# Performance work log

Measured on AMD Instinct MI355X. Metric: run time of the kernel, lower is better.

## Reference

```python
import jax, jax.numpy as jnp
import numpy as np

B, S, DIM = 2, 2048, 2048
N_HEADS, N_KV_HEADS = 32, 8
HEAD_DIM = DIM // N_HEADS  # 64
N_REP = N_HEADS // N_KV_HEADS  # 4
ROPE_THETA = 10000.0


def setup_inputs() -> dict:
    key = jax.random.key(0)
    ks = jax.random.split(key, 5)
    x = jax.random.normal(ks[0], (B, S, DIM), dtype=jnp.float32)
    # rope frequencies: freqs_cis[t, j] = exp(i * t * theta^(-2j/head_dim))
    inv_freq = 1.0 / (ROPE_THETA ** (jnp.arange(0, HEAD_DIM, 2, dtype=jnp.float32) / HEAD_DIM))
    angles = jnp.arange(S, dtype=jnp.float32)[:, None] * inv_freq[None, :]  # [S, HEAD_DIM//2]
    freqs_cos = jnp.cos(angles)
    freqs_sin = jnp.sin(angles)
    scale = 1.0 / np.sqrt(DIM)
    wq = jax.random.normal(ks[1], (N_HEADS * HEAD_DIM, DIM), dtype=jnp.float32) * scale
    wk = jax.random.normal(ks[2], (N_KV_HEADS * HEAD_DIM, DIM), dtype=jnp.float32) * scale
    wv = jax.random.normal(ks[3], (N_KV_HEADS * HEAD_DIM, DIM), dtype=jnp.float32) * scale
    wo = jax.random.normal(ks[4], (DIM, N_HEADS * HEAD_DIM), dtype=jnp.float32) * scale
    return {"x": x, "freqs_cos": freqs_cos, "freqs_sin": freqs_sin,
            "wq": wq, "wk": wk, "wv": wv, "wo": wo}


def _rope(t, cos, sin):
    # t: [B, S, H, D]; rotate consecutive pairs (even, odd) lanes -- complex mul.
    t = t.reshape(*t.shape[:-1], HEAD_DIM // 2, 2)
    t0, t1 = t[..., 0], t[..., 1]
    c = cos[None, :, None, :]  # [1, S, 1, D//2]
    s = sin[None, :, None, :]
    r0 = t0 * c - t1 * s
    r1 = t0 * s + t1 * c
    return jnp.stack([r0, r1], axis=-1).reshape(*t0.shape[:-1], HEAD_DIM)


def reference(x, freqs_cos, freqs_sin, wq, wk, wv, wo):
    bsz, seqlen, _ = x.shape
    xq = jnp.einsum('bsd,hd->bsh', x, wq).reshape(bsz, seqlen, N_HEADS, HEAD_DIM)
    xk = jnp.einsum('bsd,hd->bsh', x, wk).reshape(bsz, seqlen, N_KV_HEADS, HEAD_DIM)
    xv = jnp.einsum('bsd,hd->bsh', x, wv).reshape(bsz, seqlen, N_KV_HEADS, HEAD_DIM)
    xq = _rope(xq, freqs_cos[:seqlen], freqs_sin[:seqlen])
    xk = _rope(xk, freqs_cos[:seqlen], freqs_sin[:seqlen])
    # GQA: repeat_interleave kv heads to n_heads
    xk = jnp.repeat(xk, N_REP, axis=2)
    xv = jnp.repeat(xv, N_REP, axis=2)
    # [B, H, S, D]
    q = xq.transpose(0, 2, 1, 3)
    k = xk.transpose(0, 2, 1, 3)
    v = xv.transpose(0, 2, 1, 3)
    scores = jnp.einsum('bhqd,bhkd->bhqk', q, k) / np.sqrt(HEAD_DIM)
    causal = jnp.tril(jnp.ones((seqlen, seqlen), dtype=bool))
    scores = jnp.where(causal[None, None], scores, jnp.finfo(scores.dtype).min)
    attn = jax.nn.softmax(scores, axis=-1)
    out = jnp.einsum('bhqk,bhkd->bhqd', attn, v)
    out = out.transpose(0, 2, 1, 3).reshape(bsz, seqlen, N_HEADS * HEAD_DIM)
    return jnp.einsum('bsh,dh->bsd', out, wo)
```

## Files before the change

### kernel.cpp

```cpp
#include <hip/hip_runtime.h>
#include <hip/hip_bf16.h>
#include <stdint.h>

#define BATCH 2
#define SEQ   2048
#define DIM   2048
#define NH    32
#define NKV   8
#define HD    64
#define QKVN  3072
#define MROWS 4096

typedef __bf16 bf16x8 __attribute__((ext_vector_type(8)));
typedef float  f32x4  __attribute__((ext_vector_type(4)));
typedef unsigned short ushort8v __attribute__((ext_vector_type(8)));

typedef __attribute__((address_space(3))) void lds_void;
typedef const __attribute__((address_space(1))) void gbl_void;

__device__ __forceinline__ void gload_lds16(const void* g, void* l) {
    __builtin_amdgcn_global_load_lds((gbl_void*)g, (lds_void*)l, 16, 0, 0);
}

__global__ void cvt_f32_bf16(const float* __restrict__ in,
                             __hip_bfloat16* __restrict__ out, int n) {
    int i = (blockIdx.x * 256 + threadIdx.x) * 4;
    if (i >= n) return;
    const float4 v = *reinterpret_cast<const float4*>(in + i);
    union { ushort4 u; __hip_bfloat16 h[4]; } o;
    o.h[0] = __float2bfloat16(v.x);
    o.h[1] = __float2bfloat16(v.y);
    o.h[2] = __float2bfloat16(v.z);
    o.h[3] = __float2bfloat16(v.w);
    *reinterpret_cast<ushort4*>(out + i) = o.u;
}

__device__ __forceinline__ void store_out(float* p, float v) { *p = v; }
__device__ __forceinline__ void store_out(__hip_bfloat16* p, float v) { *p = __float2bfloat16(v); }

template <typename OUT_T>
__global__ __launch_bounds__(256) void gemm_bt(
    const __hip_bfloat16* __restrict__ A,
    const __hip_bfloat16* __restrict__ B,
    OUT_T* __restrict__ C,
    int M, int N, int K)
{
    __shared__ __align__(16) __hip_bfloat16 As[128 * 32];
    __shared__ __align__(16) __hip_bfloat16 Bs[128 * 32];
    const int tid  = threadIdx.x;
    const int lane = tid & 63;
    const int wave = tid >> 6;
    const int wr = wave >> 1, wc = wave & 1;
    const int lr = lane & 15, lg = lane >> 4;

    const int nwg = (int)(gridDim.x * gridDim.y);
    const int id  = (int)blockIdx.y * (int)gridDim.x + (int)blockIdx.x;
    const int cpx = nwg >> 3;
    const int sw  = (id & 7) * cpx + (id >> 3);
    const size_t tm = (size_t)(sw % (int)gridDim.x) * 128;
    const size_t tn = (size_t)(sw / (int)gridDim.x) * 128;

    f32x4 acc[4][4] = {};

    const int srow  = tid >> 2;
    const int scol  = (tid & 3) * 8;
    const int wbase = wave * 512;

    const __hip_bfloat16* pa = As + (wr * 64 + lr) * 32 + lg * 8;
    const __hip_bfloat16* pb = Bs + (wc * 64 + lr) * 32 + lg * 8;

    for (int k0 = 0; k0 < K; k0 += 32) {
        const __hip_bfloat16* gA = A + (tm + srow) * (size_t)K + k0 + scol;
        const __hip_bfloat16* gB = B + (tn + srow) * (size_t)K + k0 + scol;
        gload_lds16(gA,                 (void*)(As + wbase));
        gload_lds16(gA + (size_t)64*K,  (void*)(As + 2048 + wbase));
        gload_lds16(gB,                 (void*)(Bs + wbase));
        gload_lds16(gB + (size_t)64*K,  (void*)(Bs + 2048 + wbase));
        __syncthreads();
        bf16x8 af[4], bfr[4];
        #pragma unroll
        for (int m = 0; m < 4; ++m) af[m]  = *reinterpret_cast<const bf16x8*>(pa + m * 512);
        #pragma unroll
        for (int n = 0; n < 4; ++n) bfr[n] = *reinterpret_cast<const bf16x8*>(pb + n * 512);
        #pragma unroll
        for (int m = 0; m < 4; ++m)
            #pragma unroll
            for (int n = 0; n < 4; ++n)
                acc[m][n] = __builtin_amdgcn_mfma_f32_16x16x32_bf16(af[m], bfr[n], acc[m][n], 0, 0, 0);
        __syncthreads();
    }

    #pragma unroll
    for (int m = 0; m < 4; ++m)
        #pragma unroll
        for (int n = 0; n < 4; ++n)
            #pragma unroll
            for (int r = 0; r < 4; ++r) {
                size_t row = tm + wr * 64 + m * 16 + lg * 4 + r;
                size_t col = tn + wc * 64 + n * 16 + lr;
                store_out(&C[row * (size_t)N + col], acc[m][n][r]);
            }
}

__global__ void rope_qk(const __hip_bfloat16* __restrict__ qkv,
                        const float* __restrict__ fcos,
                        const float* __restrict__ fsin,
                        __hip_bfloat16* __restrict__ outp,
                        int nheads, int col_off, float mul) {
    int idx = blockIdx.x * 256 + threadIdx.x;
    int i  = idx & 31;
    int s  = (idx >> 5) & (SEQ - 1);
    int bh = idx >> 16;
    int h  = bh % nheads;
    const __hip_bfloat16* src = qkv + ((size_t)(bh / nheads) * SEQ + s) * QKVN
                                    + col_off + h * HD + 2 * i;
    union { unsigned int u; __hip_bfloat16 h2[2]; } in_, out_;
    in_.u = *reinterpret_cast<const unsigned int*>(src);
    float t0 = __bfloat162float(in_.h2[0]);
    float t1 = __bfloat162float(in_.h2[1]);
    float c  = fcos[s * 32 + i] * mul;
    float sn = fsin[s * 32 + i] * mul;
    out_.h2[0] = __float2bfloat16(t0 * c - t1 * sn);
    out_.h2[1] = __float2bfloat16(t0 * sn + t1 * c);
    *reinterpret_cast<unsigned int*>(outp + ((size_t)bh * SEQ + s) * HD + 2 * i) = out_.u;
}

__global__ __launch_bounds__(256) void v_repack(const __hip_bfloat16* __restrict__ qkv,
                                                __hip_bfloat16* __restrict__ vt) {
    __shared__ unsigned short tile[64][66];
    int blk = blockIdx.x;
    int st = blk & 31;
    int kh = (blk >> 5) & 7;
    int b  = blk >> 8;
    int s0 = st * 64;
    int t  = threadIdx.x;
    int r  = t >> 2;
    #pragma unroll
    for (int it = 0; it < 2; ++it) {
        int chunk = (t & 3) + it * 4;
        const __hip_bfloat16* src = qkv + ((size_t)(b * SEQ + s0 + r)) * QKVN
                                        + 2560 + kh * HD + chunk * 8;
        ushort8v v = *reinterpret_cast<const ushort8v*>(src);
        #pragma unroll
        for (int j = 0; j < 8; ++j) tile[r][chunk * 8 + j] = v[j];
    }
    __syncthreads();
    int d = t >> 2;
    #pragma unroll
    for (int it = 0; it < 2; ++it) {
        int chunk = (t & 3) + it * 4;
        ushort8v w;
        #pragma unroll
        for (int j = 0; j < 8; ++j) w[j] = tile[chunk * 8 + j][d];
        *reinterpret_cast<ushort8v*>(vt + ((size_t)(b * NKV + kh) * HD + d) * SEQ
                                        + s0 + chunk * 8) = w;
    }
}

__device__ __forceinline__ unsigned pack_bf16x2(float lo, float hi) {
    __hip_bfloat162 t;
    t.x = __float2bfloat16(lo);
    t.y = __float2bfloat16(hi);
    return *reinterpret_cast<unsigned*>(&t);
}

__global__ __launch_bounds__(256, 4) void flash_attn(
    const __hip_bfloat16* __restrict__ Qp,
    const __hip_bfloat16* __restrict__ Kp,
    const __hip_bfloat16* __restrict__ Vt,
    __hip_bfloat16* __restrict__ O) {
    __shared__ __align__(16) __hip_bfloat16 Kst[2][4096];
    __shared__ __align__(16) __hip_bfloat16 Vst[2][4096];
    __shared__ __align__(16) unsigned char Plds[4][2048];
    const int qt   = (int)gridDim.x - 1 - (int)blockIdx.x;
    const int bh   = blockIdx.y;
    const int b    = bh >> 5, h = bh & 31;
    const int kvh  = h >> 2;
    const int tid  = threadIdx.x;
    const int wave = tid >> 6, lane = tid & 63;
    const int lr = lane & 15, lg = lane >> 4;
    const int qw0 = qt * 64 + wave * 16;

    const __hip_bfloat16* qbase = Qp + (((size_t)bh) * SEQ + qw0 + lr) * HD + lg * 8;
    const bf16x8 qa0 = *reinterpret_cast<const bf16x8*>(qbase);
    const bf16x8 qa1 = *reinterpret_cast<const bf16x8*>(qbase + 32);

    const __hip_bfloat16* kb = Kp + ((size_t)(b * NKV + kvh) * SEQ) * HD;
    const __hip_bfloat16* vb = Vt + ((size_t)(b * NKV + kvh) * HD) * SEQ;

    const int srow = tid >> 3;
    const int sch  = (tid & 7) ^ (srow & 7);
    const size_t koff0 = (size_t)srow        * HD  + sch * 8;
    const size_t koff1 = (size_t)(srow + 32) * HD  + sch * 8;
    const size_t voff0 = (size_t)srow        * SEQ + sch * 8;
    const size_t voff1 = (size_t)(srow + 32) * SEQ + sch * 8;
    const int wvb = wave * 1024;

    int foff[4][2];
    #pragma unroll
    for (int g = 0; g < 4; ++g)
        #pragma unroll
        for (int c = 0; c < 2; ++c)
            foff[g][c] = (g * 16 + lr) * 64 + (((c * 4 + lg) ^ (lr & 7)) * 8);

    f32x4 acc[4] = {};
    float m_run = -1e30f;
    float l_run = 0.f;

    unsigned char* pw = &Plds[wave][0];
    const int swz = (lr & 7) << 4;
    const int kv_end = qt * 64 + 64;

    {
        char* kd = (char*)&Kst[0][0];
        char* vd = (char*)&Vst[0][0];
        gload_lds16(kb + koff0, kd + wvb);
        gload_lds16(kb + koff1, kd + 4096 + wvb);
        gload_lds16(vb + voff0, vd + wvb);
        gload_lds16(vb + voff1, vd + 4096 + wvb);
    }
    int cur = 0;

    for (int kv0 = 0; kv0 < kv_end; kv0 += 64) {
        __syncthreads();
        if (kv0 + 64 < kv_end) {
            const __hip_bfloat16* ks = kb + (size_t)(kv0 + 64) * HD;
            const __hip_bfloat16* vs = vb + (kv0 + 64);
            char* kd = (char*)&Kst[cur ^ 1][0];
            char* vd = (char*)&Vst[cur ^ 1][0];
            gload_lds16(ks + koff0, kd + wvb);
            gload_lds16(ks + koff1, kd + 4096 + wvb);
            gload_lds16(vs + voff0, vd + wvb);
            gload_lds16(vs + voff1, vd + 4096 + wvb);
        }
        const __hip_bfloat16* Kl = &Kst[cur][0];
        const __hip_bfloat16* Vl = &Vst[cur][0];

        f32x4 s[4];
        #pragma unroll
        for (int nk = 0; nk < 4; ++nk) {
            bf16x8 k0 = *reinterpret_cast<const bf16x8*>(Kl + foff[nk][0]);
            bf16x8 k1 = *reinterpret_cast<const bf16x8*>(Kl + foff[nk][1]);
            f32x4 z = {0.f, 0.f, 0.f, 0.f};
            z = __builtin_amdgcn_mfma_f32_16x16x32_bf16(k0, qa0, z, 0, 0, 0);
            z = __builtin_amdgcn_mfma_f32_16x16x32_bf16(k1, qa1, z, 0, 0, 0);
            s[nk] = z;
        }
        if (kv0 + 64 >= kv_end) {
            const int qg = qw0 + lr;
            #pragma unroll
            for (int nk = 0; nk < 4; ++nk) {
                const int kbase = kv0 + nk * 16 + lg * 4;
                #pragma unroll
                for (int r = 0; r < 4; ++r)
                    if (kbase + r > qg) s[nk][r] = -1e30f;
            }
        }
        float pmax = fmaxf(fmaxf(s[0][0], s[0][1]), fmaxf(s[0][2], s[0][3]));
        #pragma unroll
        for (int nk = 1; nk < 4; ++nk)
            pmax = fmaxf(pmax, fmaxf(fmaxf(s[nk][0], s[nk][1]), fmaxf(s[nk][2], s[nk][3])));
        if (!__all(pmax - m_run <= 8.0f)) {
            float tmax = fmaxf(pmax, __shfl_xor(pmax, 16, 64));
            tmax = fmaxf(tmax, __shfl_xor(tmax, 32, 64));
            const float mn    = fmaxf(m_run, tmax);
            const float alpha = __expf(m_run - mn);
            m_run = mn;
            l_run *= alpha;
            const float a0 = __shfl(alpha, lg * 4 + 0, 64);
            const float a1 = __shfl(alpha, lg * 4 + 1, 64);
            const float a2 = __shfl(alpha, lg * 4 + 2, 64);
            const float a3 = __shfl(alpha, lg * 4 + 3, 64);
            #pragma unroll
            for (int nd = 0; nd < 4; ++nd) {
                acc[nd][0] *= a0; acc[nd][1] *= a1;
                acc[nd][2] *= a2; acc[nd][3] *= a3;
            }
        }
        float tsum = 0.f;
        #pragma unroll
        for (int nk = 0; nk < 4; ++nk) {
            float p0 = __expf(s[nk][0] - m_run);
            float p1 = __expf(s[nk][1] - m_run);
            float p2 = __expf(s[nk][2] - m_run);
            float p3 = __expf(s[nk][3] - m_run);
            tsum += (p0 + p1) + (p2 + p3);
            uint2 pk;
            pk.x = pack_bf16x2(p0, p1);
            pk.y = pack_bf16x2(p2, p3);
            *reinterpret_cast<uint2*>(pw + lr * 128 + ((nk * 32 + lg * 8) ^ swz)) = pk;
        }
        l_run += tsum;
        asm volatile("s_waitcnt lgkmcnt(0)" ::: "memory");
        __builtin_amdgcn_sched_barrier(0);
        const bf16x8 pa0 = *reinterpret_cast<const bf16x8*>(pw + lr * 128 + ((     lg * 16) ^ swz));
        const bf16x8 pa1 = *reinterpret_cast<const bf16x8*>(pw + lr * 128 + ((64 + lg * 16) ^ swz));
        #pragma unroll
        for (int nd = 0; nd < 4; ++nd) {
            bf16x8 v0 = *reinterpret_cast<const bf16x8*>(Vl + foff[nd][0]);
            bf16x8 v1 = *reinterpret_cast<const bf16x8*>(Vl + foff[nd][1]);
            acc[nd] = __builtin_amdgcn_mfma_f32_16x16x32_bf16(pa0, v0, acc[nd], 0, 0, 0);
            acc[nd] = __builtin_amdgcn_mfma_f32_16x16x32_bf16(pa1, v1, acc[nd], 0, 0, 0);
        }
        cur ^= 1;
    }
    float lt = l_run;
    lt += __shfl_xor(lt, 16, 64);
    lt += __shfl_xor(lt, 32, 64);
    float linv[4];
    #pragma unroll
    for (int r = 0; r < 4; ++r)
        linv[r] = 1.f / __shfl(lt, lg * 4 + r, 64);
    #pragma unroll
    for (int nd = 0; nd < 4; ++nd)
        #pragma unroll
        for (int r = 0; r < 4; ++r) {
            int qg  = qw0 + lg * 4 + r;
            int col = h * HD + nd * 16 + lr;
            O[((size_t)(b * SEQ + qg)) * DIM + col] = __float2bfloat16(acc[nd][r] * linv[r]);
        }
}

extern "C" void kernel_launch(void* const* d_in, const int* in_sizes, int n_in,
                              void* d_out, int out_size, void* d_ws, size_t ws_size,
                              hipStream_t stream) {
    const float* x    = (const float*)d_in[0];
    const float* fcos = (const float*)d_in[1];
    const float* fsin = (const float*)d_in[2];
    const float* wq   = (const float*)d_in[3];
    const float* wk   = (const float*)d_in[4];
    const float* wv   = (const float*)d_in[5];
    const float* wo   = (const float*)d_in[6];
    float* out = (float*)d_out;

    __hip_bfloat16* Xb   = (__hip_bfloat16*)d_ws;
    __hip_bfloat16* Wqkv = Xb   + (size_t)MROWS * DIM;
    __hip_bfloat16* Wob  = Wqkv + (size_t)QKVN * DIM;
    __hip_bfloat16* QKV  = Wob  + (size_t)DIM * DIM;
    __hip_bfloat16* Qp   = QKV  + (size_t)MROWS * QKVN;
    __hip_bfloat16* Kp   = Qp   + (size_t)BATCH * NH * SEQ * HD;
    __hip_bfloat16* Vt   = Kp   + (size_t)BATCH * NKV * SEQ * HD;
    __hip_bfloat16* AO   = Xb;

    cvt_f32_bf16<<<(MROWS * DIM) / 1024, 256, 0, stream>>>(x, Xb, MROWS * DIM);
    cvt_f32_bf16<<<(DIM * DIM) / 1024, 256, 0, stream>>>(wq, Wqkv, DIM * DIM);
    cvt_f32_bf16<<<(NKV * HD * DIM) / 1024, 256, 0, stream>>>(wk, Wqkv + (size_t)DIM * DIM, NKV * HD * DIM);
    cvt_f32_bf16<<<(NKV * HD * DIM) / 1024, 256, 0, stream>>>(wv, Wqkv + (size_t)(DIM + NKV * HD) * DIM, NKV * HD * DIM);
    cvt_f32_bf16<<<(DIM * DIM) / 1024, 256, 0, stream>>>(wo, Wob, DIM * DIM);

    gemm_bt<__hip_bfloat16><<<dim3(MROWS / 128, QKVN / 128), 256, 0, stream>>>(
        Xb, Wqkv, QKV, MROWS, QKVN, DIM);

    rope_qk<<<(BATCH * NH * SEQ * 32) / 256, 256, 0, stream>>>(QKV, fcos, fsin, Qp, NH, 0, 0.125f);
    rope_qk<<<(BATCH * NKV * SEQ * 32) / 256, 256, 0, stream>>>(QKV, fcos, fsin, Kp, NKV, DIM, 1.0f);
    v_repack<<<BATCH * NKV * 32, 256, 0, stream>>>(QKV, Vt);

    flash_attn<<<dim3(SEQ / 64, BATCH * NH), 256, 0, stream>>>(Qp, Kp, Vt, AO);

    gemm_bt<float><<<dim3(MROWS / 128, DIM / 128), 256, 0, stream>>>(
        AO, Wob, out, MROWS, DIM, DIM);
}
```

Baseline: 371.5 us.

## Double-buffer GEMM LDS tiles and merge conversion and rope launches

The GEMM now uses two LDS buffers, so the next K tile is loaded with global_load_lds while the current one feeds the MFMAs, and it needs only one barrier per iteration. The four weight-conversion launches are merged into one kernel, and the Q and K rope launches into one, to cut launch overhead. The single barrier relies on the async LDS loads being complete and visible at the next __syncthreads. Doubling LDS per block may also lower occupancy.

```diff
diff --git a/kernel.cpp b/kernel.cpp
--- a/kernel.cpp
+++ b/kernel.cpp
@@ -22,17 +22,39 @@
     __builtin_amdgcn_global_load_lds((gbl_void*)g, (lds_void*)l, 16, 0, 0);
 }
 
-__global__ void cvt_f32_bf16(const float* __restrict__ in,
-                             __hip_bfloat16* __restrict__ out, int n) {
-    int i = (blockIdx.x * 256 + threadIdx.x) * 4;
-    if (i >= n) return;
-    const float4 v = *reinterpret_cast<const float4*>(in + i);
+__device__ __forceinline__ void cvt4(const float* src, __hip_bfloat16* dst) {
+    const float4 v = *reinterpret_cast<const float4*>(src);
     union { ushort4 u; __hip_bfloat16 h[4]; } o;
     o.h[0] = __float2bfloat16(v.x);
     o.h[1] = __float2bfloat16(v.y);
     o.h[2] = __float2bfloat16(v.z);
     o.h[3] = __float2bfloat16(v.w);
-    *reinterpret_cast<ushort4*>(out + i) = o.u;
+    *reinterpret_cast<ushort4*>(dst) = o.u;
+}
+
+__global__ void cvt_f32_bf16(const float* __restrict__ in,
+                             __hip_bfloat16* __restrict__ out, int n) {
+    int i = (blockIdx.x * 256 + threadIdx.x) * 4;
+    if (i >= n) return;
+    cvt4(in + i, out + i);
+}
+
+__global__ void cvt_weights(const float* __restrict__ wq,
+                            const float* __restrict__ wk,
+                            const float* __restrict__ wv,
+                            const float* __restrict__ wo,
+                            __hip_bfloat16* __restrict__ out) {
+    const int E0 = DIM * DIM;
+    const int E1 = E0 + NKV * HD * DIM;
+    const int E2 = E1 + NKV * HD * DIM;
+    int i = (blockIdx.x * 256 + threadIdx.x) * 4;
+    const float* src;
+    int off;
+    if      (i < E0) { src = wq; off = i; }
+    else if (i < E1) { src = wk; off = i - E0; }
+    else if (i < E2) { src = wv; off = i - E1; }
+    else             { src = wo; off = i - E2; }
+    cvt4(src + off, out + i);
 }
 
 __device__ __forceinline__ void store_out(float* p, float v) { *p = v; }
@@ -45,8 +67,8 @@
     OUT_T* __restrict__ C,
     int M, int N, int K)
 {
-    __shared__ __align__(16) __hip_bfloat16 As[128 * 32];
-    __shared__ __align__(16) __hip_bfloat16 Bs[128 * 32];
+    __shared__ __align__(16) __hip_bfloat16 As[2][128 * 32];
+    __shared__ __align__(16) __hip_bfloat16 Bs[2][128 * 32];
     const int tid  = threadIdx.x;
     const int lane = tid & 63;
     const int wave = tid >> 6;
@@ -66,17 +88,25 @@
     const int scol  = (tid & 3) * 8;
     const int wbase = wave * 512;
 
-    const __hip_bfloat16* pa = As + (wr * 64 + lr) * 32 + lg * 8;
-    const __hip_bfloat16* pb = Bs + (wc * 64 + lr) * 32 + lg * 8;
+    const __hip_bfloat16* gA0 = A + (tm + srow) * (size_t)K + scol;
+    const __hip_bfloat16* gB0 = B + (tn + srow) * (size_t)K + scol;
+
+    gload_lds16(gA0,                 (void*)(As[0] + wbase));
+    gload_lds16(gA0 + (size_t)64*K,  (void*)(As[0] + 2048 + wbase));
+    gload_lds16(gB0,                 (void*)(Bs[0] + wbase));
+    gload_lds16(gB0 + (size_t)64*K,  (void*)(Bs[0] + 2048 + wbase));
+    int cur = 0;
 
     for (int k0 = 0; k0 < K; k0 += 32) {
-        const __hip_bfloat16* gA = A + (tm + srow) * (size_t)K + k0 + scol;
-        const __hip_bfloat16* gB = B + (tn + srow) * (size_t)K + k0 + scol;
-        gload_lds16(gA,                 (void*)(As + wbase));
-        gload_lds16(gA + (size_t)64*K,  (void*)(As + 2048 + wbase));
-        gload_lds16(gB,                 (void*)(Bs + wbase));
-        gload_lds16(gB + (size_t)64*K,  (void*)(Bs + 2048 + wbase));
         __syncthreads();
+        if (k0 + 32 < K) {
+            gload_lds16(gA0 + k0 + 32,                (void*)(As[cur ^ 1] + wbase));
+            gload_lds16(gA0 + (size_t)64*K + k0 + 32, (void*)(As[cur ^ 1] + 2048 + wbase));
+            gload_lds16(gB0 + k0 + 32,                (void*)(Bs[cur ^ 1] + wbase));
+            gload_lds16(gB0 + (size_t)64*K + k0 + 32, (void*)(Bs[cur ^ 1] + 2048 + wbase));
+        }
+        const __hip_bfloat16* pa = As[cur] + (wr * 64 + lr) * 32 + lg * 8;
+        const __hip_bfloat16* pb = Bs[cur] + (wc * 64 + lr) * 32 + lg * 8;
         bf16x8 af[4], bfr[4];
         #pragma unroll
         for (int m = 0; m < 4; ++m) af[m]  = *reinterpret_cast<const bf16x8*>(pa + m * 512);
@@ -87,7 +117,7 @@
             #pragma unroll
             for (int n = 0; n < 4; ++n)
                 acc[m][n] = __builtin_amdgcn_mfma_f32_16x16x32_bf16(af[m], bfr[n], acc[m][n], 0, 0, 0);
-        __syncthreads();
+        cur ^= 1;
     }
 
     #pragma unroll
@@ -102,12 +132,16 @@
             }
 }
 
-__global__ void rope_qk(const __hip_bfloat16* __restrict__ qkv,
-                        const float* __restrict__ fcos,
-                        const float* __restrict__ fsin,
-                        __hip_bfloat16* __restrict__ outp,
-                        int nheads, int col_off, float mul) {
+__global__ void rope_fused(const __hip_bfloat16* __restrict__ qkv,
+                           const float* __restrict__ fcos,
+                           const float* __restrict__ fsin,
+                           __hip_bfloat16* __restrict__ Qp,
+                           __hip_bfloat16* __restrict__ Kp) {
     int idx = blockIdx.x * 256 + threadIdx.x;
+    const int QTOT = BATCH * NH * SEQ * 32;
+    int nheads, col_off; float mul; __hip_bfloat16* outp;
+    if (idx < QTOT) { nheads = NH;  col_off = 0;   mul = 0.125f; outp = Qp; }
+    else { idx -= QTOT; nheads = NKV; col_off = DIM; mul = 1.0f; outp = Kp; }
     int i  = idx & 31;
     int s  = (idx >> 5) & (SEQ - 1);
     int bh = idx >> 16;
@@ -343,16 +377,13 @@
     __hip_bfloat16* AO   = Xb;
 
     cvt_f32_bf16<<<(MROWS * DIM) / 1024, 256, 0, stream>>>(x, Xb, MROWS * DIM);
-    cvt_f32_bf16<<<(DIM * DIM) / 1024, 256, 0, stream>>>(wq, Wqkv, DIM * DIM);
-    cvt_f32_bf16<<<(NKV * HD * DIM) / 1024, 256, 0, stream>>>(wk, Wqkv + (size_t)DIM * DIM, NKV * HD * DIM);
-    cvt_f32_bf16<<<(NKV * HD * DIM) / 1024, 256, 0, stream>>>(wv, Wqkv + (size_t)(DIM + NKV * HD) * DIM, NKV * HD * DIM);
-    cvt_f32_bf16<<<(DIM * DIM) / 1024, 256, 0, stream>>>(wo, Wob, DIM * DIM);
+    cvt_weights<<<(QKVN * DIM + DIM * DIM) / 1024, 256, 0, stream>>>(wq, wk, wv, wo, Wqkv);
 
     gemm_bt<__hip_bfloat16><<<dim3(MROWS / 128, QKVN / 128), 256, 0, stream>>>(
         Xb, Wqkv, QKV, MROWS, QKVN, DIM);
 
-    rope_qk<<<(BATCH * NH * SEQ * 32) / 256, 256, 0, stream>>>(QKV, fcos, fsin, Qp, NH, 0, 0.125f);
-    rope_qk<<<(BATCH * NKV * SEQ * 32) / 256, 256, 0, stream>>>(QKV, fcos, fsin, Kp, NKV, DIM, 1.0f);
+    rope_fused<<<(BATCH * (NH + NKV) * SEQ * 32) / 256, 256, 0, stream>>>(
+        QKV, fcos, fsin, Qp, Kp);
     v_repack<<<BATCH * NKV * 32, 256, 0, stream>>>(QKV, Vt);
 
     flash_attn<<<dim3(SEQ / 64, BATCH * NH), 256, 0, stream>>>(Qp, Kp, Vt, AO);
```

Measured after the change: 355.1 us. 1.05x faster.
